# Optimization experiments

Measured on AMD Instinct MI355X. Metric: run time of the kernel, lower is better.

## Reference

```python
import jax, jax.numpy as jnp
import numpy as np
from jax import lax

B, N, T, H, E, V, F = 16, 5, 10, 512, 250, 30000, 2048  # N must be num_layers*num_dirs+1 = 5


def setup_inputs() -> dict:
    key = jax.random.key(0)
    ks = jax.random.split(key, 20)
    s = 0.05
    def rn(k, shp):
        return jax.random.normal(k, shp, jnp.float32) * s
    z = lambda n: jnp.zeros((n,), jnp.float32)
    return {
        "img": jax.random.normal(ks[0], (B, F), jnp.float32),
        "caps": jax.random.randint(ks[1], (B, N, T), 0, V, dtype=jnp.int32),
        "Wh1": rn(ks[2], (F, 2 * H)), "bh1": z(2 * H),
        "Wh2": rn(ks[3], (2 * H, H)), "bh2": z(H),
        "Wc1": rn(ks[4], (F, 2 * H)), "bc1": z(2 * H),
        "Wc2": rn(ks[5], (2 * H, H)), "bc2": z(H),
        "emb": rn(ks[6], (V, E)),
        "Wih0f": rn(ks[7], (E, 4 * H)), "Whh0f": rn(ks[8], (H, 4 * H)), "b0f": z(4 * H),
        "Wih0b": rn(ks[9], (E, 4 * H)), "Whh0b": rn(ks[10], (H, 4 * H)), "b0b": z(4 * H),
        "Wih1f": rn(ks[11], (2 * H, 4 * H)), "Whh1f": rn(ks[12], (H, 4 * H)), "b1f": z(4 * H),
        "Wih1b": rn(ks[13], (2 * H, 4 * H)), "Whh1b": rn(ks[14], (H, 4 * H)), "b1b": z(4 * H),
        "Wfc": rn(ks[15], (2 * H, V)), "bfc": z(V),
    }


def _lstm_dir(x, h0, c0, Wih, Whh, b, reverse):
    # x: [t, B, in]; PyTorch gate order i, f, g, o
    xs = x[::-1] if reverse else x
    xg = xs @ Wih + b  # precomputed input projection [t, B, 4H]
    def step(carry, xg_t):
        h, c = carry
        g = xg_t + h @ Whh
        i, f, gg, o = jnp.split(g, 4, axis=-1)
        c = jax.nn.sigmoid(f) * c + jax.nn.sigmoid(i) * jnp.tanh(gg)
        h = jax.nn.sigmoid(o) * jnp.tanh(c)
        return (h, c), h
    (hT, cT), hs = lax.scan(step, (h0, c0), xg)
    if reverse:
        hs = hs[::-1]
    return hs, hT, cT


def _bilstm2(x, h0, c0, p):
    # 2-layer bidirectional LSTM; state layout [l0_fwd, l0_bwd, l1_fwd, l1_bwd]
    of, hf0, cf0 = _lstm_dir(x, h0[0], c0[0], *p[0], False)
    ob, hb0, cb0 = _lstm_dir(x, h0[1], c0[1], *p[1], True)
    x1 = jnp.concatenate([of, ob], axis=-1)  # [t, B, 2H]
    o1f, hf1, cf1 = _lstm_dir(x1, h0[2], c0[2], *p[2], False)
    o1b, hb1, cb1 = _lstm_dir(x1, h0[3], c0[3], *p[3], True)
    out = jnp.concatenate([o1f, o1b], axis=-1)  # [t, B, 2H]
    hN = jnp.stack([hf0, hb0, hf1, hb1])
    cN = jnp.stack([cf0, cb0, cf1, cb1])
    return out, hN, cN


def _forward(img, caps, Wh1, bh1, Wh2, bh2, Wc1, bc1, Wc2, bc2, emb,
             Wih0f, Whh0f, b0f, Wih0b, Whh0b, b0b,
             Wih1f, Whh1f, b1f, Wih1b, Whh1b, b1b, Wfc, bfc):
    relu = jax.nn.relu
    h = relu(relu(img @ Wh1 + bh1) @ Wh2 + bh2)  # init_h MLP (dropout = identity in eval)
    c = relu(relu(img @ Wc1 + bc1) @ Wc2 + bc2)  # init_c MLP
    hs = jnp.broadcast_to(h[None], (N - 1, B, H))  # N-1 == 4 == num_layers*num_dirs
    cs = jnp.broadcast_to(c[None], (N - 1, B, H))
    seq = jnp.transpose(emb[caps], (1, 2, 0, 3))  # [N, T, B, E] caption-major prefixes
    p = ((Wih0f, Whh0f, b0f), (Wih0b, Whh0b, b0b),
         (Wih1f, Whh1f, b1f), (Wih1b, Whh1b, b1b))
    outs = None
    # Faithful reproduction of the original's redundant prefix recomputation:
    # at each outer step t, the LSTM is re-run on every caption's length-(t+1)
    # prefix, chaining (h, c) across captions; only the final step's outputs
    # survive, but the state chain depends on all prior iterations.
    for t in range(T):
        outs_t = []
        for n in range(N):
            o, hs, cs = _bilstm2(seq[n, :t + 1], hs, cs, p)
            outs_t.append(o)
        outs = outs_t
    out = jnp.stack(outs)  # [N, T, B, 2H]
    return out @ Wfc + bfc  # logits [N, T, B, V]


def reference(img, caps, Wh1, bh1, Wh2, bh2, Wc1, bc1, Wc2, bc2, emb,
              Wih0f, Whh0f, b0f, Wih0b, Whh0b, b0b,
              Wih1f, Whh1f, b1f, Wih1b, Whh1b, b1b, Wfc, bfc):
    return _forward(img, caps, Wh1, bh1, Wh2, bh2, Wc1, bc1, Wc2, bc2, emb,
                    Wih0f, Whh0f, b0f, Wih0b, Whh0b, b0b,
                    Wih1f, Whh1f, b1f, Wih1b, Whh1b, b1b, Wfc, bfc)
```

## Files before the change

### kernel.cpp

```cpp
#include <hip/hip_runtime.h>

typedef unsigned short u16;
typedef unsigned int   u32;
typedef unsigned long long u64;
typedef __attribute__((ext_vector_type(8))) short s8v;
typedef __attribute__((ext_vector_type(4))) float f4v;

#define DEVI __device__ __forceinline__

#define B_  16
#define N_  5
#define T_  10
#define H_  512
#define E_  250
#define V_  30000
#define F_  2048
#define FH  2048
#define H2  1024
#define NCOMP 128

__device__ u32   g_flag;
__device__ u32   g_slot0[NCOMP];
__device__ u32   g_slot1[NCOMP];
__device__ __attribute__((aligned(64))) u16   g_H0[4*2*16*512];
__device__ __attribute__((aligned(64))) u16   g_H1[4*2*16*512];
__device__ __attribute__((aligned(64))) float g_cinit[16*512];
__device__ __attribute__((aligned(64))) u16   g_A1[2*2*16*1024];
__device__ __attribute__((aligned(64))) u16   g_X1[4*2*10*16*1024];
__device__ __attribute__((aligned(64))) u16   g_OUT1[2*800*1024];
__device__ __attribute__((aligned(64))) u16   g_TOK[800*256];

DEVI f4v MFMA(s8v a, s8v b, f4v c){ return __builtin_amdgcn_mfma_f32_16x16x32_bf16(a,b,c,0,0,0); }
DEVI float bf2f(u16 u){ union{u32 i; float f;} v; v.i = ((u32)u)<<16; return v.f; }
DEVI u16 f2bf(float f){ union{float f; u32 i;} v; v.f = f; u32 i = v.i + 0x7fffu + ((v.i>>16)&1u); return (u16)(i>>16); }
DEVI float sigm(float x){ return 1.0f/(1.0f+__expf(-x)); }
DEVI float tanhfast(float x){ float e = __expf(2.0f*x); return 1.0f - 2.0f/(e+1.0f); }

DEVI s8v ld16(const u16* p){ return *(const s8v*)p; }
DEVI s8v ld16u(const u16* p){ s8v a; __builtin_memcpy(&a, p, 16); return a; }

DEVI void ldc(s8v& d, const u16* p){
  asm volatile("global_load_dwordx4 %0, %1, off sc0 sc1" : "=v"(d) : "v"(p));
}
template<int N> DEVI void waitv(s8v& a){
  asm volatile("s_waitcnt vmcnt(%1)" : "+v"(a) : "n"(N));
}
template<int N> DEVI void waitv2(s8v& a, s8v& b){
  asm volatile("s_waitcnt vmcnt(%2)" : "+v"(a), "+v"(b) : "n"(N));
}

DEVI void st2c(u16* p, u16 v){
  asm volatile("global_store_short %0, %1, off sc0 sc1" :: "v"(p), "v"((u32)v) : "memory");
}

DEVI u16 ldw(const void* W, size_t idx, int f32){
  return f32 ? f2bf(((const float*)W)[idx]) : ((const u16*)W)[idx];
}
DEVI float ldwf(const void* W, size_t idx, int f32){
  return f32 ? ((const float*)W)[idx] : bf2f(((const u16*)W)[idx]);
}
DEVI s8v ldA8(const void* A, size_t idx, int f32){
  if(f32){
    const float* p = (const float*)A + idx;
    s8v a;
    #pragma unroll
    for(int j=0;j<8;++j) a[j] = (short)f2bf(p[j]);
    return a;
  }
  return ld16u((const u16*)A + idx);
}
DEVI s8v gatherBf(const void* W, int ld, int row0, int col, int f32){
  s8v r;
  #pragma unroll
  for(int j=0;j<8;++j) r[j] = (short)ldw(W, (size_t)(row0+j)*ld + col, f32);
  return r;
}

#define RPT4(M,b)  M(b) M((b)+1) M((b)+2) M((b)+3)
#define RPT8(M,b)  RPT4(M,b) RPT4(M,(b)+4)
#define RPT16(M,b) RPT8(M,b) RPT8(M,(b)+8)

DEVI void publish_slot(u32* slot, u32 val){
  asm volatile("s_waitcnt vmcnt(0)" ::: "memory");
  if((threadIdx.x & 63)==0)
    __hip_atomic_store(slot, val, __ATOMIC_RELAXED, __HIP_MEMORY_SCOPE_SYSTEM);
}
DEVI void poll_n64(u32* base, u32 tgt){
  int l = threadIdx.x & 63;
  for(;;){
    u32 a = __hip_atomic_load(&base[l], __ATOMIC_RELAXED, __HIP_MEMORY_SCOPE_SYSTEM);
    if(__all((int)(a>=tgt))) break;
    __builtin_amdgcn_s_sleep(1);
  }
  asm volatile("s_waitcnt vmcnt(0)" ::: "memory");
}
DEVI void poll_n128(u32* base, u32 tgt){
  int l = threadIdx.x & 63;
  for(;;){
    u32 a = __hip_atomic_load(&base[l],    __ATOMIC_RELAXED, __HIP_MEMORY_SCOPE_SYSTEM);
    u32 b = __hip_atomic_load(&base[l+64], __ATOMIC_RELAXED, __HIP_MEMORY_SCOPE_SYSTEM);
    if(__all((int)(a>=tgt && b>=tgt))) break;
    __builtin_amdgcn_s_sleep(1);
  }
  asm volatile("s_waitcnt vmcnt(0)" ::: "memory");
}

__global__ __launch_bounds__(64) void k0(const void* img){
  int l = threadIdx.x;
  const u16* p = (const u16*)img;
  int bad = 0;
  #pragma unroll
  for(int i=0;i<4;++i){
    float v = bf2f(p[l + 64*i]);
    if(!(fabsf(v) <= 1e4f)) bad = 1;
  }
  unsigned long long mb = __ballot(bad);
  g_slot0[l] = 0u; g_slot0[l+64] = 0u;
  g_slot1[l] = 0u; g_slot1[l+64] = 0u;
  if(l==0){ g_flag = (mb != 0ull) ? 1u : 0u; }
}

__global__ __launch_bounds__(256) void k_tok(const int* caps, const void* emb){
  int f32 = (int)g_flag;
  int idx = blockIdx.x*256 + threadIdx.x;
  int bnr = idx>>8, e = idx&255;
  int tok = caps[bnr];
  u16 v = (e < E_) ? ldw(emb, (size_t)tok*E_ + e, f32) : (u16)0;
  g_TOK[idx] = v;
}

__global__ __launch_bounds__(256) void k1a(const void* img, const void* Wh1, const void* bh1,
                                           const void* Wc1, const void* bc1){
  int f32 = (int)g_flag;
  int w = threadIdx.x>>6, l = threadIdx.x&63, q = l>>4, c = l&15, m = l&15;
  int widx = blockIdx.x*4 + w;
  int which = widx>>6;
  int ct    = widx&63;
  const void* W    = which? Wc1 : Wh1;
  const void* bias = which? bc1 : bh1;
  int col = ct*16 + c;
  f4v acc = {0.f,0.f,0.f,0.f};
  for(int kc=0; kc<64; ++kc){
    s8v a = ldA8(img, (size_t)m*F_ + kc*32 + q*8, f32);
    s8v b = gatherBf(W, H2, kc*32+q*8, col, f32);
    acc = MFMA(a,b,acc);
  }
  float bi = ldwf(bias, col, f32);
  #pragma unroll
  for(int r=0;r<4;++r){
    float v = fmaxf(acc[r]+bi, 0.f);
    u16 hi = f2bf(v); u16 lo = f2bf(v - bf2f(hi));
    int rowb = q*4+r;
    g_A1[(size_t)(which*2+0)*B_*H2 + (size_t)rowb*H2 + col] = hi;
    g_A1[(size_t)(which*2+1)*B_*H2 + (size_t)rowb*H2 + col] = lo;
  }
}

__global__ __launch_bounds__(256) void k1b(const void* Wh2, const void* bh2,
                                           const void* Wc2, const void* bc2){
  int f32 = (int)g_flag;
  int w = threadIdx.x>>6, l = threadIdx.x&63, q = l>>4, c = l&15, m = l&15;
  int widx = blockIdx.x*4 + w;
  int which = widx>>5;
  int ct    = widx&31;
  const void* W    = which? Wc2 : Wh2;
  const void* bias = which? bc2 : bh2;
  const u16* Ab    = g_A1 + (size_t)which*2*B_*H2;
  int col = ct*16 + c;
  f4v acc = {0.f,0.f,0.f,0.f};
  for(int kc=0; kc<32; ++kc){
    s8v ah = ld16(Ab + (size_t)m*H2 + kc*32 + q*8);
    s8v al = ld16(Ab + (size_t)B_*H2 + (size_t)m*H2 + kc*32 + q*8);
    s8v b  = gatherBf(W, H_, kc*32+q*8, col, f32);
    acc = MFMA(ah,b,acc);
    acc = MFMA(al,b,acc);
  }
  float bi = ldwf(bias, col, f32);
  #pragma unroll
  for(int r=0;r<4;++r){
    float v = fmaxf(acc[r]+bi, 0.f);
    int rowb = q*4+r;
    if(which==0){
      u16 hi = f2bf(v); u16 lo = f2bf(v - bf2f(hi));
      #pragma unroll
      for(int dir=0; dir<2; ++dir){
        size_t base = (size_t)(dir*2+0)*16384;
        g_H0[base + 0*8192 + rowb*512 + col] = hi;  g_H0[base + 1*8192 + rowb*512 + col] = lo;
        g_H1[base + 0*8192 + rowb*512 + col] = hi;  g_H1[base + 1*8192 + rowb*512 + col] = lo;
      }
    } else {
      g_cinit[(size_t)rowb*H_ + col] = v;
    }
  }
}

DEVI float gate_combine(f4v acc, float& cs, int l){
  int base = (l & 48) | (l & 3);
  int sel  = (l >> 2) & 3;
  float G[4];
  #pragma unroll
  for(int gg=0; gg<4; ++gg){
    int src = base | (gg<<2);
    float a0 = __shfl(acc[0], src, 64);
    float a1 = __shfl(acc[1], src, 64);
    float a2 = __shfl(acc[2], src, 64);
    float a3 = __shfl(acc[3], src, 64);
    float x = (sel&1)? a1 : a0;
    float y = (sel&1)? a3 : a2;
    G[gg] = (sel&2)? y : x;
  }
  float iG = sigm(G[0]);
  float fG = sigm(G[1]);
  float gG = tanhfast(G[2]);
  float oG = sigm(G[3]);
  cs = fG*cs + iG*gG;
  return oG * tanhfast(cs);
}

__global__ __launch_bounds__(128) void k2(const void* Wih0f, const void* Whh0f, const void* b0f,
                                          const void* Wih0b, const void* Whh0b, const void* b0b,
                                          const void* Wih1f, const void* Whh1f, const void* b1f,
                                          const void* Wih1b, const void* Whh1b, const void* b1b){
  __shared__ u16 sw[2*24576];
  int tid = threadIdx.x;
  int blk = blockIdx.x;
  int f32 = (int)g_flag;
  int wv  = tid>>6;
  int l   = tid&63;
  int q = l>>4, c = l&15, m = l&15;
  int dir = blk>>6; int blkd = blk&63;
  int hb  = blkd*8;
  int gc0 = (c>>2)*512 + hb + (c&3);
  int gc1 = gc0 + 4;
  int bo  = q*4 + (c>>2);
  int hc0 = hb + (c&3), hc1 = hc0 + 4;

  const void* Wih0 = dir? Wih0b : Wih0f;
  const void* Whh0 = dir? Whh0b : Whh0f;
  const void* b0   = dir? b0b   : b0f;
  const void* Wih1 = dir? Wih1b : Wih1f;
  const void* Whh1 = dir? Whh1b : Whh1f;
  const void* b1   = dir? b1b   : b1f;

  for(int tt=0; tt<2; ++tt){
    int gb = hb + tt*4;
    for(int ii=tid; ii<24576; ii+=128){
      int kc=ii>>9, rem=ii&511, cc=rem>>5, qq=(rem>>3)&3, j=ii&7;
      int gc = (cc>>2)*512 + gb + (cc&3);
      int rowk = kc*32+qq*8+j;
      sw[tt*24576+ii] = (rowk < H2) ? ldw(Wih1, (size_t)rowk*FH + gc, f32)
                                    : ldw(Whh1, (size_t)(rowk-H2)*FH + gc, f32);
    }
  }

  s8v w0a[16], w0b[16], wxa[8], wxb[8];
  float cA0=0.f, cA1=0.f, biasA0=0.f, biasA1=0.f;
  float cB0=0.f, cB1=0.f, biasB0=0.f, biasB1=0.f;
  if(wv==0){
    #pragma unroll
    for(int kc=0;kc<16;++kc){
      #pragma unroll
      for(int j=0;j<8;++j){
        int rowk = kc*32+q*8+j;
        w0a[kc][j] = (short)ldw(Whh0, (size_t)rowk*FH + gc0, f32);
        w0b[kc][j] = (short)ldw(Whh0, (size_t)rowk*FH + gc1, f32);
      }
    }
    #pragma unroll
    for(int kc=0;kc<8;++kc){
      #pragma unroll
      for(int j=0;j<8;++j){
        int rowk = kc*32+q*8+j;
        wxa[kc][j] = (rowk<E_)? (short)ldw(Wih0, (size_t)rowk*FH + gc0, f32) : (short)0;
        wxb[kc][j] = (rowk<E_)? (short)ldw(Wih0, (size_t)rowk*FH + gc1, f32) : (short)0;
      }
    }
    biasA0 = ldwf(b0, gc0, f32); biasA1 = ldwf(b0, gc1, f32);
    cA0 = g_cinit[(size_t)bo*H_ + hc0]; cA1 = g_cinit[(size_t)bo*H_ + hc1];
  } else {
    biasB0 = ldwf(b1, gc0, f32); biasB1 = ldwf(b1, gc1, f32);
    cB0 = g_cinit[(size_t)bo*H_ + hc0]; cB1 = g_cinit[(size_t)bo*H_ + hc1];
  }
  __syncthreads();

  if(wv==0){
    u32 i0 = 0; int p0 = 0;
    for(int k=0; k<50; ++k){
      int Lk = k/5 + 1; int n0 = k - (k/5)*5;
      if(k>=4){
        u32 need = 0;
        for(int j=0;j<k-3;++j) need += (u32)(j/5+1);
        poll_n128(g_slot1, need);
      }
      for(int s=0; s<Lk; ++s){
        int row = dir ? (Lk-1-s) : s;
        const u16* er = g_TOK + ((size_t)(m*N_ + n0)*T_ + row)*256;
        const u16* Hr = g_H0 + (size_t)(dir*2 + p0)*16384;
        f4v A0 = {biasA0,biasA0,biasA0,biasA0};
        f4v A1 = {biasA1,biasA1,biasA1,biasA1};
        #pragma unroll
        for(int kc=0;kc<8;++kc){
          s8v a = ld16(er + kc*32 + q*8);
          A0 = MFMA(a, wxa[kc], A0); A1 = MFMA(a, wxb[kc], A1);
        }
        poll_n64(g_slot0 + dir*64, i0);
        s8v hst[16];
#define H0ISS(f) ldc(hst[(f)], Hr + (((f)&1)?8192u:0u) + (size_t)m*H_ + (((f)>>1)*32) + q*8);
#define H0STEP(f) { \
        waitv<(((f)<16)?15:(31-(f)))>(hst[(f)&15]); \
        A0 = MFMA(hst[(f)&15], w0a[(f)>>1], A0); \
        A1 = MFMA(hst[(f)&15], w0b[(f)>>1], A1); \
        if((f)+16<32) ldc(hst[(f)&15], Hr + (((f)&1)?8192u:0u) + (size_t)m*H_ + (((((f)+16))>>1)*32) + q*8); }
        RPT16(H0ISS,0)
        RPT16(H0STEP,0) RPT16(H0STEP,16)
        float hn0 = gate_combine(A0, cA0, l);
        float hn1 = gate_combine(A1, cA1, l);
        u16 h0h=f2bf(hn0), h0l=f2bf(hn0 - bf2f(h0h));
        u16 h1h=f2bf(hn1), h1l=f2bf(hn1 - bf2f(h1h));
        u16* Hw = g_H0 + (size_t)(dir*2 + (p0^1))*16384;
        st2c(Hw + (size_t)bo*H_ + hc0, h0h); st2c(Hw + 8192 + (size_t)bo*H_ + hc0, h0l);
        st2c(Hw + (size_t)bo*H_ + hc1, h1h); st2c(Hw + 8192 + (size_t)bo*H_ + hc1, h1l);
        u16* Xw = g_X1 + (size_t)(k&3)*327680;
        size_t xr = ((size_t)row*16 + bo)*H2 + dir*H_;
        st2c(Xw + xr + hc0, h0h); st2c(Xw + 163840 + xr + hc0, h0l);
        st2c(Xw + xr + hc1, h1h); st2c(Xw + 163840 + xr + hc1, h1l);
        publish_slot(&g_slot0[blk], i0+1);
        ++i0; p0 ^= 1;
      }
    }
  } else {
    u32 i1 = 0, Sc = 0; int p1 = 0;
    for(int cl=0; cl<50; ++cl){
      int Lc = cl/5 + 1; int n1 = cl - (cl/5)*5;
      poll_n128(g_slot0, Sc + (u32)Lc);
      for(int s=0; s<Lc; ++s){
        int row = dir ? (Lc-1-s) : s;
        const u16* Xr  = g_X1 + (size_t)(cl&3)*327680 + ((size_t)row*16)*H2;
        const u16* Xr2 = Xr + 163840;
        const u16* Hr1 = g_H1 + (size_t)(dir*2 + p1)*16384;
        f4v A0 = {biasB0,biasB0,biasB0,biasB0};
        f4v A1 = {biasB1,biasB1,biasB1,biasB1};
        s8v sh[12], sl[12];
#define XISS(kc) { ldc(sh[(kc)], Xr + (size_t)m*H2 + ((kc)*32) + q*8); \
                   ldc(sl[(kc)], Xr2 + (size_t)m*H2 + ((kc)*32) + q*8); }
#define XSTEP(kc) { \
        waitv2<(((kc)<20)?22:(62-2*(kc)))>(sh[(kc)%12], sl[(kc)%12]); \
        s8v bf0 = ld16(sw + (kc)*512 + c*32 + q*8); \
        s8v bf1 = ld16(sw + 24576 + (kc)*512 + c*32 + q*8); \
        A0 = MFMA(sh[(kc)%12], bf0, A0); A0 = MFMA(sl[(kc)%12], bf0, A0); \
        A1 = MFMA(sh[(kc)%12], bf1, A1); A1 = MFMA(sl[(kc)%12], bf1, A1); \
        if((kc)+12<32){ ldc(sh[(kc)%12], Xr + (size_t)m*H2 + (((kc)+12)*32) + q*8); \
                        ldc(sl[(kc)%12], Xr2 + (size_t)m*H2 + (((kc)+12)*32) + q*8); } }
        RPT8(XISS,0) RPT4(XISS,8)
        RPT16(XSTEP,0) RPT16(XSTEP,16)
        poll_n64(g_slot1 + dir*64, i1);
#define H1ISS(h) { ldc(sh[(h)], Hr1 + (size_t)m*H_ + ((h)*32) + q*8); \
                   ldc(sl[(h)], Hr1 + 8192 + (size_t)m*H_ + ((h)*32) + q*8); }
#define H1STEP(h) { \
        waitv2<(((h)<4)?22:(30-2*(h)))>(sh[(h)%12], sl[(h)%12]); \
        s8v bf0 = ld16(sw + (32+(h))*512 + c*32 + q*8); \
        s8v bf1 = ld16(sw + 24576 + (32+(h))*512 + c*32 + q*8); \
        A0 = MFMA(sh[(h)%12], bf0, A0); A0 = MFMA(sl[(h)%12], bf0, A0); \
        A1 = MFMA(sh[(h)%12], bf1, A1); A1 = MFMA(sl[(h)%12], bf1, A1); \
        if((h)+12<16){ ldc(sh[(h)%12], Hr1 + (size_t)m*H_ + (((h)+12)*32) + q*8); \
                       ldc(sl[(h)%12], Hr1 + 8192 + (size_t)m*H_ + (((h)+12)*32) + q*8); } }
        RPT8(H1ISS,0) RPT4(H1ISS,8)
        RPT16(H1STEP,0)
        float hn0 = gate_combine(A0, cB0, l);
        float hn1 = gate_combine(A1, cB1, l);
        u16 h0h=f2bf(hn0), h0l=f2bf(hn0 - bf2f(h0h));
        u16 h1h=f2bf(hn1), h1l=f2bf(hn1 - bf2f(h1h));
        u16* Hw = g_H1 + (size_t)(dir*2 + (p1^1))*16384;
        st2c(Hw + (size_t)bo*H_ + hc0, h0h); st2c(Hw + 8192 + (size_t)bo*H_ + hc0, h0l);
        st2c(Hw + (size_t)bo*H_ + hc1, h1h); st2c(Hw + 8192 + (size_t)bo*H_ + hc1, h1l);
        size_t orow = (size_t)(n1*10 + row)*16 + bo;
        st2c(g_OUT1 + orow*H2 + dir*H_ + hc0, h0h);
        st2c(g_OUT1 + (size_t)800*H2 + orow*H2 + dir*H_ + hc0, h0l);
        st2c(g_OUT1 + orow*H2 + dir*H_ + hc1, h1h);
        st2c(g_OUT1 + (size_t)800*H2 + orow*H2 + dir*H_ + hc1, h1l);
        publish_slot(&g_slot1[blk], i1+1);
        ++i1; p1 ^= 1;
      }
      Sc += (u32)Lc;
    }
  }
}

__global__ __launch_bounds__(256,1) void k3(const void* Wfc, const void* bfc, void* out){
  int f32 = (int)g_flag;
  int w = threadIdx.x>>6, l = threadIdx.x&63, q = l>>4, c = l&15, m = l&15;
  int ct = blockIdx.x*4 + w;
  if(ct >= 1875) return;
  int col = ct*16 + c;
  s8v bfr[32];
  #pragma unroll
  for(int kc=0; kc<32; ++kc){
    #pragma unroll
    for(int j=0;j<8;++j) bfr[kc][j] = (short)ldw(Wfc, (size_t)(kc*32+q*8+j)*V_ + col, f32);
  }
  float bi = ldwf(bfc, col, f32);
  for(int rt=0; rt<50; ++rt){
    f4v acc = {0.f,0.f,0.f,0.f};
    const u16* Ah = g_OUT1 + (size_t)(rt*16 + m)*H2;
    const u16* Al = Ah + (size_t)800*H2;
    #pragma unroll
    for(int kc=0; kc<32; ++kc){
      acc = MFMA(ld16(Ah + kc*32 + q*8), bfr[kc], acc);
      acc = MFMA(ld16(Al + kc*32 + q*8), bfr[kc], acc);
    }
    if(f32){
      float* o = (float*)out;
      #pragma unroll
      for(int r=0;r<4;++r) o[(size_t)(rt*16 + q*4 + r)*V_ + col] = acc[r] + bi;
    } else {
      u16* o = (u16*)out;
      #pragma unroll
      for(int r=0;r<4;++r) o[(size_t)(rt*16 + q*4 + r)*V_ + col] = f2bf(acc[r] + bi);
    }
  }
}

extern "C" void kernel_launch(void* const* d_in, const int* in_sizes, int n_in,
                              void* d_out, int out_size, void* d_ws, size_t ws_size,
                              hipStream_t stream){
  (void)in_sizes; (void)n_in; (void)out_size; (void)d_ws; (void)ws_size;
  const void* img  = d_in[0];
  const int*  caps = (const int*)d_in[1];
  const void* Wh1=d_in[2],  *bh1=d_in[3];
  const void* Wh2=d_in[4],  *bh2=d_in[5];
  const void* Wc1=d_in[6],  *bc1=d_in[7];
  const void* Wc2=d_in[8],  *bc2=d_in[9];
  const void* emb=d_in[10];
  const void* Wih0f=d_in[11], *Whh0f=d_in[12], *b0f=d_in[13];
  const void* Wih0b=d_in[14], *Whh0b=d_in[15], *b0b=d_in[16];
  const void* Wih1f=d_in[17], *Whh1f=d_in[18], *b1f=d_in[19];
  const void* Wih1b=d_in[20], *Whh1b=d_in[21], *b1b=d_in[22];
  const void* Wfc=d_in[23],  *bfc=d_in[24];

  hipLaunchKernelGGL(k0,    dim3(1),     dim3(64),  0, stream, img);
  hipLaunchKernelGGL(k_tok, dim3(800),   dim3(256), 0, stream, caps, emb);
  hipLaunchKernelGGL(k1a,   dim3(32),    dim3(256), 0, stream, img, Wh1, bh1, Wc1, bc1);
  hipLaunchKernelGGL(k1b,   dim3(16),    dim3(256), 0, stream, Wh2, bh2, Wc2, bc2);
  hipLaunchKernelGGL(k2,    dim3(NCOMP), dim3(128), 0, stream,
                     Wih0f, Whh0f, b0f, Wih0b, Whh0b, b0b,
                     Wih1f, Whh1f, b1f, Wih1b, Whh1b, b1b);
  hipLaunchKernelGGL(k3,    dim3(469),   dim3(256), 0, stream, Wfc, bfc, d_out);
}
```

Before: 3.682 ms.

## Overlap layer-1 input projection with recurrent wait and publish slots earlier

In the layer-1 wave, the input-projection MFMAs for the next timestep now run right after the current step's hidden state is published. This moves them off the critical path between polling for peer hidden states and the recurrent matmul. The layer-0 wave publishes its slot before writing X1 on non-final steps, and layer-1 publishes before writing outputs, so dependent blocks are released sooner. The change also reindexes the LDS weight layout to a lane*8 stride, shrinks the X prefetch ring to 8, and adds unroll pragmas to the head GEMMs. Publishing a slot before the X1 stores risks a consumer reading stale data unless ordering is guaranteed elsewhere. The final-step guard suggests only the last row is consumed cross-block.

```diff
diff --git a/kernel.cpp b/kernel.cpp
--- a/kernel.cpp
+++ b/kernel.cpp
@@ -140,6 +140,7 @@
   const void* bias = which? bc1 : bh1;
   int col = ct*16 + c;
   f4v acc = {0.f,0.f,0.f,0.f};
+  #pragma unroll 4
   for(int kc=0; kc<64; ++kc){
     s8v a = ldA8(img, (size_t)m*F_ + kc*32 + q*8, f32);
     s8v b = gatherBf(W, H2, kc*32+q*8, col, f32);
@@ -168,6 +169,7 @@
   const u16* Ab    = g_A1 + (size_t)which*2*B_*H2;
   int col = ct*16 + c;
   f4v acc = {0.f,0.f,0.f,0.f};
+  #pragma unroll 4
   for(int kc=0; kc<32; ++kc){
     s8v ah = ld16(Ab + (size_t)m*H2 + kc*32 + q*8);
     s8v al = ld16(Ab + (size_t)B_*H2 + (size_t)m*H2 + kc*32 + q*8);
@@ -228,6 +230,7 @@
   int wv  = tid>>6;
   int l   = tid&63;
   int q = l>>4, c = l&15, m = l&15;
+  int l8 = l*8;
   int dir = blk>>6; int blkd = blk&63;
   int hb  = blkd*8;
   int gc0 = (c>>2)*512 + hb + (c&3);
@@ -245,7 +248,10 @@
   for(int tt=0; tt<2; ++tt){
     int gb = hb + tt*4;
     for(int ii=tid; ii<24576; ii+=128){
-      int kc=ii>>9, rem=ii&511, cc=rem>>5, qq=(rem>>3)&3, j=ii&7;
+      int kc = ii>>9;
+      int lane = (ii>>3)&63;
+      int j  = ii&7;
+      int cc = lane&15, qq = lane>>4;
       int gc = (cc>>2)*512 + gb + (cc&3);
       int rowk = kc*32+qq*8+j;
       sw[tt*24576+ii] = (rowk < H2) ? ldw(Wih1, (size_t)rowk*FH + gc, f32)
@@ -322,48 +328,58 @@
         st2c(Hw + (size_t)bo*H_ + hc1, h1h); st2c(Hw + 8192 + (size_t)bo*H_ + hc1, h1l);
         u16* Xw = g_X1 + (size_t)(k&3)*327680;
         size_t xr = ((size_t)row*16 + bo)*H2 + dir*H_;
-        st2c(Xw + xr + hc0, h0h); st2c(Xw + 163840 + xr + hc0, h0l);
-        st2c(Xw + xr + hc1, h1h); st2c(Xw + 163840 + xr + hc1, h1l);
-        publish_slot(&g_slot0[blk], i0+1);
+        if(s==Lk-1){
+          st2c(Xw + xr + hc0, h0h); st2c(Xw + 163840 + xr + hc0, h0l);
+          st2c(Xw + xr + hc1, h1h); st2c(Xw + 163840 + xr + hc1, h1l);
+          publish_slot(&g_slot0[blk], i0+1);
+        } else {
+          publish_slot(&g_slot0[blk], i0+1);
+          st2c(Xw + xr + hc0, h0h); st2c(Xw + 163840 + xr + hc0, h0l);
+          st2c(Xw + xr + hc1, h1h); st2c(Xw + 163840 + xr + hc1, h1l);
+        }
         ++i0; p0 ^= 1;
       }
     }
   } else {
     u32 i1 = 0, Sc = 0; int p1 = 0;
-    for(int cl=0; cl<50; ++cl){
-      int Lc = cl/5 + 1; int n1 = cl - (cl/5)*5;
-      poll_n128(g_slot0, Sc + (u32)Lc);
-      for(int s=0; s<Lc; ++s){
-        int row = dir ? (Lc-1-s) : s;
-        const u16* Xr  = g_X1 + (size_t)(cl&3)*327680 + ((size_t)row*16)*H2;
-        const u16* Xr2 = Xr + 163840;
-        const u16* Hr1 = g_H1 + (size_t)(dir*2 + p1)*16384;
-        f4v A0 = {biasB0,biasB0,biasB0,biasB0};
-        f4v A1 = {biasB1,biasB1,biasB1,biasB1};
-        s8v sh[12], sl[12];
-#define XISS(kc) { ldc(sh[(kc)], Xr + (size_t)m*H2 + ((kc)*32) + q*8); \
-                   ldc(sl[(kc)], Xr2 + (size_t)m*H2 + ((kc)*32) + q*8); }
-#define XSTEP(kc) { \
-        waitv2<(((kc)<20)?22:(62-2*(kc)))>(sh[(kc)%12], sl[(kc)%12]); \
-        s8v bf0 = ld16(sw + (kc)*512 + c*32 + q*8); \
-        s8v bf1 = ld16(sw + 24576 + (kc)*512 + c*32 + q*8); \
-        A0 = MFMA(sh[(kc)%12], bf0, A0); A0 = MFMA(sl[(kc)%12], bf0, A0); \
-        A1 = MFMA(sh[(kc)%12], bf1, A1); A1 = MFMA(sl[(kc)%12], bf1, A1); \
-        if((kc)+12<32){ ldc(sh[(kc)%12], Xr + (size_t)m*H2 + (((kc)+12)*32) + q*8); \
-                        ldc(sl[(kc)%12], Xr2 + (size_t)m*H2 + (((kc)+12)*32) + q*8); } }
-        RPT8(XISS,0) RPT4(XISS,8)
-        RPT16(XSTEP,0) RPT16(XSTEP,16)
-        poll_n64(g_slot1 + dir*64, i1);
+    f4v A0, A1;
+    s8v sh[12], sl[12];
+#define XISS8(kc) { ldc(sh[(kc)], Xr + (size_t)m*H2 + ((kc)*32) + q*8); \
+                    ldc(sl[(kc)], Xr2 + (size_t)m*H2 + ((kc)*32) + q*8); }
+#define XSTEP8(kc) { \
+        waitv2<(((kc)<24)?14:(2*(31-(kc))))>(sh[(kc)&7], sl[(kc)&7]); \
+        s8v bf0 = ld16(sw + (kc)*512 + l8); \
+        s8v bf1 = ld16(sw + 24576 + (kc)*512 + l8); \
+        A0 = MFMA(sh[(kc)&7], bf0, A0); A0 = MFMA(sl[(kc)&7], bf0, A0); \
+        A1 = MFMA(sh[(kc)&7], bf1, A1); A1 = MFMA(sl[(kc)&7], bf1, A1); \
+        if((kc)+8<32){ ldc(sh[(kc)&7], Xr + (size_t)m*H2 + (((kc)+8)*32) + q*8); \
+                       ldc(sl[(kc)&7], Xr2 + (size_t)m*H2 + (((kc)+8)*32) + q*8); } }
+#define XPHASE(rowv) { \
+        const u16* Xr  = Xbase + ((size_t)(rowv)*16)*H2; \
+        const u16* Xr2 = Xr + 163840; \
+        A0 = (f4v){biasB0,biasB0,biasB0,biasB0}; \
+        A1 = (f4v){biasB1,biasB1,biasB1,biasB1}; \
+        RPT8(XISS8,0) \
+        RPT16(XSTEP8,0) RPT16(XSTEP8,16) }
 #define H1ISS(h) { ldc(sh[(h)], Hr1 + (size_t)m*H_ + ((h)*32) + q*8); \
                    ldc(sl[(h)], Hr1 + 8192 + (size_t)m*H_ + ((h)*32) + q*8); }
 #define H1STEP(h) { \
         waitv2<(((h)<4)?22:(30-2*(h)))>(sh[(h)%12], sl[(h)%12]); \
-        s8v bf0 = ld16(sw + (32+(h))*512 + c*32 + q*8); \
-        s8v bf1 = ld16(sw + 24576 + (32+(h))*512 + c*32 + q*8); \
+        s8v bf0 = ld16(sw + (32+(h))*512 + l8); \
+        s8v bf1 = ld16(sw + 24576 + (32+(h))*512 + l8); \
         A0 = MFMA(sh[(h)%12], bf0, A0); A0 = MFMA(sl[(h)%12], bf0, A0); \
         A1 = MFMA(sh[(h)%12], bf1, A1); A1 = MFMA(sl[(h)%12], bf1, A1); \
         if((h)+12<16){ ldc(sh[(h)%12], Hr1 + (size_t)m*H_ + (((h)+12)*32) + q*8); \
                        ldc(sl[(h)%12], Hr1 + 8192 + (size_t)m*H_ + (((h)+12)*32) + q*8); } }
+    for(int cl=0; cl<50; ++cl){
+      int Lc = cl/5 + 1; int n1 = cl - (cl/5)*5;
+      poll_n128(g_slot0, Sc + (u32)Lc);
+      const u16* Xbase = g_X1 + (size_t)(cl&3)*327680;
+      XPHASE(dir ? (Lc-1) : 0)
+      for(int s=0; s<Lc; ++s){
+        int row = dir ? (Lc-1-s) : s;
+        const u16* Hr1 = g_H1 + (size_t)(dir*2 + p1)*16384;
+        poll_n64(g_slot1 + dir*64, i1);
         RPT8(H1ISS,0) RPT4(H1ISS,8)
         RPT16(H1STEP,0)
         float hn0 = gate_combine(A0, cB0, l);
@@ -373,12 +389,13 @@
         u16* Hw = g_H1 + (size_t)(dir*2 + (p1^1))*16384;
         st2c(Hw + (size_t)bo*H_ + hc0, h0h); st2c(Hw + 8192 + (size_t)bo*H_ + hc0, h0l);
         st2c(Hw + (size_t)bo*H_ + hc1, h1h); st2c(Hw + 8192 + (size_t)bo*H_ + hc1, h1l);
+        publish_slot(&g_slot1[blk], i1+1);
+        if(s+1<Lc){ XPHASE(dir ? (Lc-2-s) : (s+1)) }
         size_t orow = (size_t)(n1*10 + row)*16 + bo;
         st2c(g_OUT1 + orow*H2 + dir*H_ + hc0, h0h);
         st2c(g_OUT1 + (size_t)800*H2 + orow*H2 + dir*H_ + hc0, h0l);
         st2c(g_OUT1 + orow*H2 + dir*H_ + hc1, h1h);
         st2c(g_OUT1 + (size_t)800*H2 + orow*H2 + dir*H_ + hc1, h1l);
-        publish_slot(&g_slot1[blk], i1+1);
         ++i1; p1 ^= 1;
       }
       Sc += (u32)Lc;
```

Measured after the change: 3.856 ms. +4.7%, slower.
